# Performance work log

Hardware: AMD Instinct MI355X
Metric: run time of the kernel (lower is better)

## Reference

```python
import jax, jax.numpy as jnp
import numpy as np
import math

B_, CIN, CH, COUT, H_, W_ = 4, 96, 96, 96, 48, 48
DSTATE, DTRANK = 16, math.ceil(CH / 16)
DI = 2 * CH


def conv2d(x, w, b=None, groups=1):
    # x: NCHW, w: OIHW, 'same' padding for odd kernels
    p = (w.shape[-1] - 1) // 2
    y = jax.lax.conv_general_dilated(x, w, (1, 1), [(p, p), (p, p)],
                                     dimension_numbers=('NCHW', 'OIHW', 'NCHW'),
                                     feature_group_count=groups)
    return y if b is None else y + b[None, :, None, None]


def layernorm_last(x, g, b, eps=1e-5):
    mu = x.mean(-1, keepdims=True)
    v = jnp.mean((x - mu) ** 2, -1, keepdims=True)
    return (x - mu) * jax.lax.rsqrt(v + eps) * g + b


def selective_scan(u, delta, A, Bs, Cs, D):
    # u, delta: (B,K,Di,L); A: (K,Di,N); Bs, Cs: (B,K,N,L); D: (K,Di)
    dt = jnp.moveaxis(delta, -1, 0)  # (L,B,K,Di)
    ut = jnp.moveaxis(u, -1, 0)
    Bt = jnp.moveaxis(Bs, -1, 0)     # (L,B,K,N)
    Ct = jnp.moveaxis(Cs, -1, 0)
    N = A.shape[-1]

    def step(h, inp):
        d, uu, bb, cc = inp
        # h: (B,K,Di,N)
        h = h * jnp.exp(d[..., None] * A) + (d * uu)[..., None] * bb[:, :, None, :]
        y = jnp.einsum('bkdn,bkn->bkd', h, cc)
        return h, y

    step = jax.checkpoint(step)
    h0 = jnp.zeros(u.shape[:3] + (N,), u.dtype)
    _, ys = jax.lax.scan(step, h0, (dt, ut, Bt, Ct))
    return jnp.moveaxis(ys, 0, -1) + u * D[None, :, :, None]


def ss2d(x, in_w, cw, cb, xpw, dtw, dtb, A_log, Dp, ong, onb, ow):
    # x: (B,H,W,C) -> (B,H,W,C)
    B, H, W, C = x.shape
    Di = in_w.shape[0] // 2
    xi, z = jnp.split(x @ in_w.T, 2, -1)
    xc = jax.nn.silu(conv2d(jnp.transpose(xi, (0, 3, 1, 2)), cw, cb, groups=Di))
    L = H * W
    xf = xc.reshape(B, Di, L)
    xwh = jnp.transpose(xc, (0, 1, 3, 2)).reshape(B, Di, L)
    xh = jnp.stack([xf, xwh], 1)                      # (B,2,Di,L)
    xs = jnp.concatenate([xh, jnp.flip(xh, -1)], 1)   # (B,4,Di,L) 4-direction cross-scan
    xdbl = jnp.einsum('bkdl,kcd->bkcl', xs, xpw)
    R = dtw.shape[-1]
    N = A_log.shape[-1]
    dts, Bs, Cs = jnp.split(xdbl, [R, R + N], axis=2)
    delta = jax.nn.softplus(jnp.einsum('bkrl,kdr->bkdl', dts, dtw) + dtb[None, :, :, None])
    A = -jnp.exp(A_log.reshape(4, Di, N))
    oy = selective_scan(xs, delta, A, Bs, Cs, Dp.reshape(4, Di))  # (B,4,Di,L)
    inv = jnp.flip(oy[:, 2:4], -1)
    why = jnp.transpose(oy[:, 1].reshape(B, Di, W, H), (0, 1, 3, 2)).reshape(B, Di, L)
    invwhy = jnp.transpose(inv[:, 1].reshape(B, Di, W, H), (0, 1, 3, 2)).reshape(B, Di, L)
    y = oy[:, 0] + inv[:, 0] + why + invwhy           # (B,Di,L)
    y = layernorm_last(jnp.transpose(y, (0, 2, 1)).reshape(B, H, W, Di), ong, onb)
    return (y * jax.nn.silu(z)) @ ow.T


def crm(x, s1, s2, gw, gb, p1, p2):
    C = x.shape[1]
    uc = C // 2
    up = conv2d(x[:, :uc], s1)
    low = conv2d(x[:, uc:], s2)
    Y1 = conv2d(up, gw, gb, groups=2) + conv2d(up, p1)
    Y2 = jnp.concatenate([conv2d(low, p2), low], 1)
    out = jnp.concatenate([Y1, Y2], 1)                # (B,2C,H,W)
    out = jax.nn.softmax(out.mean((2, 3), keepdims=True), axis=1) * out
    o1, o2 = jnp.split(out, 2, 1)
    return o1 + o2


def _forward(x, conv1_w, conv1_b, bn_g, bn_b, lin_w, lin_b, dw1_w, dw1_b, dw2_w, dw2_b, ag1_w, ag1_b, ag2_w, ag2_b, ln_g, ln_b, sq1_w, sq2_w, gwc_w, gwc_b, pwc1_w, pwc2_w, fin_w, fin_b, ss_in_w, ss_conv_w, ss_conv_b, ss_xproj_w, ss_dt_w, ss_dt_b, ss_Alog, ss_D, ss_outn_g, ss_outn_b, ss_out_w):
    C = conv1_w.shape[0]
    # conv1x1 + BatchNorm(eval: running mean 0, var 1) + ReLU
    h = conv2d(x, conv1_w, conv1_b)
    h = jax.nn.relu(h * (bn_g * jax.lax.rsqrt(jnp.float32(1.0 + 1e-5)))[None, :, None, None] + bn_b[None, :, None, None])
    # token-wise linear over channels
    t = jnp.transpose(h, (0, 2, 3, 1)) @ lin_w.T + lin_b
    h = jnp.transpose(t, (0, 3, 1, 2))
    # branch 1: DWConv -> SiLU -> SS2D
    x1 = jax.nn.silu(conv2d(h, dw1_w, dw1_b, groups=C))
    x1 = ss2d(jnp.transpose(x1, (0, 2, 3, 1)), ss_in_w, ss_conv_w, ss_conv_b,
              ss_xproj_w, ss_dt_w, ss_dt_b, ss_Alog, ss_D, ss_outn_g, ss_outn_b, ss_out_w)
    x1 = jnp.transpose(x1, (0, 3, 1, 2))
    # branch 2: DWConv -> SiLU -> AttentionGate modulation
    x2 = jax.nn.silu(conv2d(h, dw2_w, dw2_b, groups=C))
    g = jax.nn.sigmoid(conv2d(jax.nn.relu(conv2d(x2, ag1_w, ag1_b)), ag2_w, ag2_b))
    y = x1 + x2 * g
    # per-pixel channel LayerNorm
    mu = y.mean(1, keepdims=True)
    v = jnp.mean((y - mu) ** 2, 1, keepdims=True)
    y = (y - mu) * jax.lax.rsqrt(v + 1e-5) * ln_g[None, :, None, None] + ln_b[None, :, None, None]
    y = crm(y, sq1_w, sq2_w, gwc_w, gwc_b, pwc1_w, pwc2_w)
    out = jnp.transpose(y, (0, 2, 3, 1)) @ fin_w.T + fin_b
    return jnp.transpose(out, (0, 3, 1, 2))


def setup_inputs():
    key = jax.random.key(0)

    def rnd(i, shape, s=0.02):
        return (jax.random.normal(jax.random.fold_in(key, i), shape) * s).astype(jnp.float32)

    CH2, N, R = CH // 2, DSTATE, DTRANK
    inp = dict(
        x=jax.random.normal(jax.random.fold_in(key, 0), (B_, CIN, H_, W_), jnp.float32),
        conv1_w=rnd(1, (CH, CIN, 1, 1)), conv1_b=jnp.zeros((CH,), jnp.float32),
        bn_g=jnp.ones((CH,), jnp.float32), bn_b=jnp.zeros((CH,), jnp.float32),
        lin_w=rnd(2, (CH, CH)), lin_b=jnp.zeros((CH,), jnp.float32),
        dw1_w=rnd(3, (CH, 1, 3, 3)), dw1_b=jnp.zeros((CH,), jnp.float32),
        dw2_w=rnd(4, (CH, 1, 3, 3)), dw2_b=jnp.zeros((CH,), jnp.float32),
        ag1_w=rnd(5, (CH2, CH, 1, 1)), ag1_b=jnp.zeros((CH2,), jnp.float32),
        ag2_w=rnd(6, (CH, CH2, 1, 1)), ag2_b=jnp.zeros((CH,), jnp.float32),
        ln_g=jnp.ones((CH,), jnp.float32), ln_b=jnp.zeros((CH,), jnp.float32),
        sq1_w=rnd(7, (CH // 4, CH2, 1, 1)), sq2_w=rnd(8, (CH // 4, CH2, 1, 1)),
        gwc_w=rnd(9, (CH, CH // 8, 3, 3)), gwc_b=jnp.zeros((CH,), jnp.float32),
        pwc1_w=rnd(10, (CH, CH // 4, 1, 1)), pwc2_w=rnd(11, (CH - CH // 4, CH // 4, 1, 1)),
        fin_w=rnd(12, (COUT, CH)), fin_b=jnp.zeros((COUT,), jnp.float32),
        ss_in_w=rnd(13, (2 * DI, CH)),
        ss_conv_w=rnd(14, (DI, 1, 3, 3)), ss_conv_b=jnp.zeros((DI,), jnp.float32),
        ss_xproj_w=rnd(15, (4, R + 2 * N, DI)),
        ss_dt_w=rnd(16, (4, DI, R), R ** -0.5),
    )
    dt = jnp.exp(jax.random.uniform(jax.random.fold_in(key, 17), (4, DI)) *
                 (math.log(0.1) - math.log(0.001)) + math.log(0.001))
    inp['ss_dt_b'] = (dt + jnp.log(-jnp.expm1(-dt))).astype(jnp.float32)
    inp['ss_Alog'] = jnp.tile(jnp.log(jnp.arange(1, DSTATE + 1, dtype=jnp.float32))[None, :], (4 * DI, 1))
    inp['ss_D'] = jnp.ones((4 * DI,), jnp.float32)
    inp['ss_outn_g'] = jnp.ones((DI,), jnp.float32)
    inp['ss_outn_b'] = jnp.zeros((DI,), jnp.float32)
    inp['ss_out_w'] = rnd(18, (CH, DI))
    return inp


def reference(x, conv1_w, conv1_b, bn_g, bn_b, lin_w, lin_b, dw1_w, dw1_b, dw2_w, dw2_b, ag1_w, ag1_b, ag2_w, ag2_b, ln_g, ln_b, sq1_w, sq2_w, gwc_w, gwc_b, pwc1_w, pwc2_w, fin_w, fin_b, ss_in_w, ss_conv_w, ss_conv_b, ss_xproj_w, ss_dt_w, ss_dt_b, ss_Alog, ss_D, ss_outn_g, ss_outn_b, ss_out_w):
    return _forward(x, conv1_w, conv1_b, bn_g, bn_b, lin_w, lin_b, dw1_w, dw1_b, dw2_w, dw2_b, ag1_w, ag1_b, ag2_w, ag2_b, ln_g, ln_b, sq1_w, sq2_w, gwc_w, gwc_b, pwc1_w, pwc2_w, fin_w, fin_b, ss_in_w, ss_conv_w, ss_conv_b, ss_xproj_w, ss_dt_w, ss_dt_b, ss_Alog, ss_D, ss_outn_g, ss_outn_b, ss_out_w)
```

## Files before the change

kernel.cpp:

```cpp
#include <hip/hip_runtime.h>
#include <hip/hip_bf16.h>

#define Bn   4
#define CHn  96
#define Hh   48
#define Ww   48
#define Ll   2304
#define Pp   9216
#define DIn  192
#define Nn   16
#define Rr   6
#define Sseg   32
#define SEGL   72
#define NCH     9
#define HSPLIT 884736

__device__ inline float siluf(float x){ return x / (1.0f + __expf(-x)); }
__device__ inline float sigmf(float x){ return 1.0f / (1.0f + __expf(-x)); }

__device__ inline int pix_of(int k, int l){
  if (k == 0) return l;
  if (k == 1) return (l % 48) * 48 + l / 48;
  if (k == 2) return Ll - 1 - l;
  int lr = Ll - 1 - l; return (lr % 48) * 48 + lr / 48;
}
__device__ inline int l_of(int k, int p){
  if (k == 0) return p;
  if (k == 1) return (p % 48) * 48 + p / 48;
  if (k == 2) return Ll - 1 - p;
  return Ll - 1 - ((p % 48) * 48 + p / 48);
}

__device__ inline float4* hptr(float* lo, float* hi, size_t idx){
  return (float4*)(idx < HSPLIT ? lo + idx : hi + (idx - HSPLIT));
}

struct TArgs {
  const float* s[14];
  float* d[14];
  int rows[14];
  int cols[14];
};
__global__ void k_tr(TArgs a){
  int id = blockIdx.y;
  int n = a.rows[id] * a.cols[id];
  int t = blockIdx.x * blockDim.x + threadIdx.x;
  if (t < n){
    int r = t / a.cols[id];
    int c = t - r * a.cols[id];
    a.d[id][c * a.rows[id] + r] = a.s[id][t];
  }
}

__global__ __launch_bounds__(256) void k_pre(const float* __restrict__ x, const float* __restrict__ w1T, const float* __restrict__ b1,
                      const float* __restrict__ bng, const float* __restrict__ bnb,
                      const float* __restrict__ linT, const float* __restrict__ lb,
                      float* __restrict__ hlin){
  __shared__ float xv[16][97];
  __shared__ float hv[16][97];
  int tid = threadIdx.x;
  int m = tid >> 4, t = tid & 15;
  int p0 = blockIdx.x * 16;
  int b = p0 / Ll; int pp0 = p0 - b * Ll;
  #pragma unroll
  for (int it = 0; it < 6; ++it){
    int e = it * 256 + tid; int c = e >> 4; int mm = e & 15;
    xv[mm][c] = x[((size_t)(b * CHn + c)) * Ll + pp0 + mm];
  }
  __syncthreads();
  float acc[6];
  #pragma unroll
  for (int j = 0; j < 6; ++j) acc[j] = 0.f;
  for (int i = 0; i < CHn; ++i){
    float xval = xv[m][i];
    #pragma unroll
    for (int j = 0; j < 6; ++j)
      acc[j] = fmaf(w1T[i * CHn + t + 16 * j], xval, acc[j]);
  }
  #pragma unroll
  for (int j = 0; j < 6; ++j){
    int c = t + 16 * j;
    float s = bng[c] * rsqrtf(1.0f + 1e-5f);
    hv[m][c] = fmaxf((acc[j] + b1[c]) * s + bnb[c], 0.f);
  }
  __syncthreads();
  float a2[6];
  #pragma unroll
  for (int j = 0; j < 6; ++j) a2[j] = lb[t + 16 * j];
  for (int i = 0; i < CHn; ++i){
    float hval = hv[m][i];
    #pragma unroll
    for (int j = 0; j < 6; ++j)
      a2[j] = fmaf(linT[i * CHn + t + 16 * j], hval, a2[j]);
  }
  int p = p0 + m;
  #pragma unroll
  for (int j = 0; j < 6; ++j)
    hlin[(size_t)p * CHn + t + 16 * j] = a2[j];
}

__global__ void k_dw(const float* __restrict__ hlin,
                     const float* __restrict__ dw1w, const float* __restrict__ dw1b,
                     const float* __restrict__ dw2w, const float* __restrict__ dw2b,
                     float* __restrict__ x1pre, float* __restrict__ x2){
  int t = blockIdx.x * 256 + threadIdx.x;
  if (t >= Pp * CHn) return;
  int c = t % CHn; int p = t / CHn; int b = p / Ll; int pp = p - b * Ll;
  int r = pp / Ww; int cx = pp - r * Ww;
  float a1 = dw1b[c], a2 = dw2b[c];
  for (int dy = -1; dy <= 1; ++dy){
    int ny = r + dy; if ((unsigned)ny >= Hh) continue;
    for (int dx = -1; dx <= 1; ++dx){
      int nx = cx + dx; if ((unsigned)nx >= Ww) continue;
      float v = hlin[(size_t)((b * Ll) + ny * Ww + nx) * CHn + c];
      int wi = c * 9 + (dy + 1) * 3 + (dx + 1);
      a1 = fmaf(dw1w[wi], v, a1);
      a2 = fmaf(dw2w[wi], v, a2);
    }
  }
  x1pre[t] = siluf(a1);
  x2[t]   = siluf(a2);
}

__global__ __launch_bounds__(256) void k_gate(const float* __restrict__ x2,
                       const float* __restrict__ ag1T, const float* __restrict__ ag1b,
                       const float* __restrict__ ag2T, const float* __restrict__ ag2b,
                       float* __restrict__ x2g){
  __shared__ float xv[16][97];
  __shared__ float rv[16][49];
  int tid = threadIdx.x;
  int m = tid >> 4, t = tid & 15;
  int p0 = blockIdx.x * 16;
  #pragma unroll
  for (int it = 0; it < 6; ++it){
    int e = it * 256 + tid; int mm = e / 96; int c = e - mm * 96;
    xv[mm][c] = x2[(size_t)(p0 + mm) * CHn + c];
  }
  __syncthreads();
  float a[3];
  #pragma unroll
  for (int jj = 0; jj < 3; ++jj) a[jj] = ag1b[t + 16 * jj];
  for (int i = 0; i < CHn; ++i){
    float xval = xv[m][i];
    #pragma unroll
    for (int jj = 0; jj < 3; ++jj)
      a[jj] = fmaf(ag1T[i * 48 + t + 16 * jj], xval, a[jj]);
  }
  #pragma unroll
  for (int jj = 0; jj < 3; ++jj) rv[m][t + 16 * jj] = fmaxf(a[jj], 0.f);
  __syncthreads();
  float a2[6];
  #pragma unroll
  for (int j = 0; j < 6; ++j) a2[j] = ag2b[t + 16 * j];
  for (int i = 0; i < 48; ++i){
    float rval = rv[m][i];
    #pragma unroll
    for (int j = 0; j < 6; ++j)
      a2[j] = fmaf(ag2T[i * CHn + t + 16 * j], rval, a2[j]);
  }
  int p = p0 + m;
  #pragma unroll
  for (int j = 0; j < 6; ++j){
    int c = t + 16 * j;
    x2g[(size_t)p * CHn + c] = xv[m][c] * sigmf(a2[j]);
  }
}

__global__ __launch_bounds__(256) void k_ssin(const float* __restrict__ x1pre, const float* __restrict__ inT,
                                              float* __restrict__ xi, float* __restrict__ z){
  __shared__ float Xs[32][17];
  __shared__ float Wsh[32][128];
  int tid = threadIdx.x;
  int mt = blockIdx.x % 576; int nt = blockIdx.x / 576;
  int p0 = mt * 16, n0 = nt * 128;
  int tx = tid & 15, ty = tid >> 4;
  float acc[8];
  #pragma unroll
  for (int j = 0; j < 8; ++j) acc[j] = 0.f;
  for (int kc = 0; kc < 96; kc += 32){
    #pragma unroll
    for (int it = 0; it < 2; ++it){
      int e = it * 256 + tid; int dd = e & 31; int m = e >> 5;
      Xs[dd][m] = x1pre[(size_t)(p0 + m) * CHn + kc + dd];
    }
    #pragma unroll
    for (int it = 0; it < 16; ++it){
      int e = it * 256 + tid; int n = e & 127; int dd = e >> 7;
      Wsh[dd][n] = inT[(size_t)(kc + dd) * 384 + n0 + n];
    }
    __syncthreads();
    #pragma unroll
    for (int dd = 0; dd < 32; ++dd){
      float xv = Xs[dd][ty];
      #pragma unroll
      for (int j = 0; j < 8; ++j)
        acc[j] = fmaf(xv, Wsh[dd][tx + 16 * j], acc[j]);
    }
    __syncthreads();
  }
  int p = p0 + ty;
  #pragma unroll
  for (int j = 0; j < 8; ++j){
    int n = n0 + tx + 16 * j;
    float v = acc[j];
    if (n < 192) xi[(size_t)p * DIn + n] = v;
    else         z [(size_t)p * DIn + (n - 192)] = v;
  }
}

__global__ void k_ssdw(const float* __restrict__ xi, const float* __restrict__ scw,
                       const float* __restrict__ scb, float* __restrict__ xc){
  int t = blockIdx.x * 256 + threadIdx.x;
  if (t >= Pp * DIn) return;
  int d = t % DIn; int p = t / DIn; int b = p / Ll; int pp = p - b * Ll;
  int r = pp / Ww; int cx = pp - r * Ww;
  float a = scb[d];
  for (int dy = -1; dy <= 1; ++dy){
    int ny = r + dy; if ((unsigned)ny >= Hh) continue;
    for (int dx = -1; dx <= 1; ++dx){
      int nx = cx + dx; if ((unsigned)nx >= Ww) continue;
      float v = xi[(size_t)((b * Ll) + ny * Ww + nx) * DIn + d];
      a = fmaf(scw[d * 9 + (dy + 1) * 3 + (dx + 1)], v, a);
    }
  }
  xc[t] = siluf(a);
}

__global__ __launch_bounds__(256) void k_xproj(const float* __restrict__ xc,
    const float* __restrict__ xpwT, float* __restrict__ part){
  __shared__ float Xs[32][17];
  __shared__ float Wsh[32][160];
  int tid = threadIdx.x;
  int mt = blockIdx.x / 6; int kc = (blockIdx.x - mt * 6) * 32;
  int p0g = mt * 16;
  int tx = tid & 15, ty = tid >> 4;
  const float* xbase = xc + (size_t)p0g * DIn + kc;
  #pragma unroll
  for (int it = 0; it < 2; ++it){
    int e = it * 256 + tid; int dd = e & 31; int m = e >> 5;
    Xs[dd][m] = xbase[(size_t)m * DIn + dd];
  }
  #pragma unroll
  for (int it = 0; it < 20; ++it){
    int e = it * 256 + tid; int dd = e / 160; int n = e - dd * 160;
    Wsh[dd][n] = (n < 152) ? xpwT[(size_t)(kc + dd) * 152 + n] : 0.f;
  }
  __syncthreads();
  float acc[10];
  #pragma unroll
  for (int j = 0; j < 10; ++j) acc[j] = 0.f;
  #pragma unroll
  for (int dd = 0; dd < 32; ++dd){
    float xv = Xs[dd][ty];
    #pragma unroll
    for (int j = 0; j < 10; ++j)
      acc[j] = fmaf(xv, Wsh[dd][tx + 16 * j], acc[j]);
  }
  float* pb = part + ((size_t)blockIdx.x * 16 + ty) * 152;
  #pragma unroll
  for (int j = 0; j < 10; ++j){
    int n = tx + 16 * j;
    if (n < 152) pb[n] = acc[j];
  }
}

__global__ void k_xred(const float* __restrict__ part, float* __restrict__ bc,
                       float* __restrict__ dtsG){
  int t = blockIdx.x * 256 + threadIdx.x;
  if (t >= Pp * 152) return;
  int p = t / 152, n = t - p * 152;
  int mt = p >> 4, m = p & 15;
  const float* pb = part + ((size_t)(mt * 6) * 16 + m) * 152 + n;
  float s = 0.f;
  #pragma unroll
  for (int kc = 0; kc < 6; ++kc) s += pb[(size_t)kc * 16 * 152];
  int b = p / Ll; int pp = p - b * Ll;
  int k = n / 38, jj = n - k * 38;
  int l = l_of(k, pp);
  if (jj < 6) dtsG[((size_t)((b * 4 + k) * Ll + l)) * 6 + jj] = s;
  else        bc [((size_t)((b * 4 + k) * Ll + l)) * 32 + (jj - 6)] = s;
}

__global__ void k_pack(const float* __restrict__ dtsG, const float* __restrict__ dtwT,
                       const float* __restrict__ dtb, const float* __restrict__ xc,
                       float* __restrict__ packed){
  int t = blockIdx.x * 256 + threadIdx.x;
  if (t >= 36864 * DIn) return;
  int d = t % DIn; int row = t / DIn;
  int bk = row / Ll; int l = row - bk * Ll;
  int k = bk & 3; int b = bk >> 2;
  const float* ds = dtsG + (size_t)row * 6;
  float a = dtb[k * DIn + d];
  #pragma unroll
  for (int r = 0; r < 6; ++r)
    a = fmaf(dtwT[r * 768 + k * DIn + d], ds[r], a);
  float dt = fmaxf(a, 0.f) + __logf(1.0f + __expf(-fabsf(a)));
  int pix = pix_of(k, l);
  float u = xc[((size_t)(b * Ll) + pix) * DIn + d];
  int unit = bk * 12 + (d >> 4);
  size_t base = ((size_t)unit * Ll + l) * 32 + (d & 15);
  packed[base]      = dt;
  packed[base + 16] = dt * u;
}


__global__ __launch_bounds__(64) void k_scanA(const float* __restrict__ packed, const float* __restrict__ bc,
                                              const float* __restrict__ Alog,
                                              float* __restrict__ hend, float* __restrict__ dtsum){
  int blk = blockIdx.x; int unit = blk >> 5; int seg = blk & 31;
  int g = unit % 12; int bk = unit / 12; int k = bk & 3;
  int lane = threadIdx.x; int ch = lane >> 2; int ns = lane & 3; int nb = ns * 4;
  int d = g * 16 + ch;
  const int arow = (k * DIn + d) * 16 + nb;
  float A0 = -__expf(Alog[arow + 0]);
  float A1 = -__expf(Alog[arow + 1]);
  float A2 = -__expf(Alog[arow + 2]);
  float A3 = -__expf(Alog[arow + 3]);
  float h0 = 0.f, h1 = 0.f, h2 = 0.f, h3 = 0.f, dacc = 0.f;

  const int l0 = seg * SEGL;
  const float* pbase = packed + ((size_t)unit * Ll + l0) * 32;
  const float* bbase = bc + ((size_t)(bk * Ll) + l0) * 32;

  __shared__ float pl[256];
  __shared__ float blA[128];

  float4 pn = *(const float4*)(pbase + lane * 4);
  float4 bn;
  if (lane < 32) bn = *(const float4*)(bbase + (size_t)(lane >> 2) * 32 + (lane & 3) * 4);
  *(float4*)&pl[lane * 4] = pn;
  if (lane < 32) *(float4*)&blA[lane * 4] = bn;
  __syncthreads();

  for (int cc = 0; cc < NCH; ++cc){
    bool more = (cc + 1 < NCH);
    if (more){
      pn = *(const float4*)(pbase + (cc + 1) * 256 + lane * 4);
      if (lane < 32) bn = *(const float4*)(bbase + (size_t)((cc + 1) * 8 + (lane >> 2)) * 32 + (lane & 3) * 4);
    }
    #pragma unroll
    for (int lp = 0; lp < 8; ++lp){
      float dt = pl[lp * 32 + ch];
      float du = pl[lp * 32 + 16 + ch];
      float4 Bv = *(const float4*)&blA[lp * 16 + nb];
      dacc += dt;
      h0 = fmaf(h0, __expf(dt * A0), du * Bv.x);
      h1 = fmaf(h1, __expf(dt * A1), du * Bv.y);
      h2 = fmaf(h2, __expf(dt * A2), du * Bv.z);
      h3 = fmaf(h3, __expf(dt * A3), du * Bv.w);
    }
    __syncthreads();
    if (more){
      *(float4*)&pl[lane * 4] = pn;
      if (lane < 32) *(float4*)&blA[lane * 4] = bn;
    }
    __syncthreads();
  }
  size_t sb = (size_t)unit * Sseg + seg;
  *(float4*)&hend[sb * 256 + lane * 4] = make_float4(h0, h1, h2, h3);
  if (ns == 0) dtsum[sb * 16 + ch] = dacc;
}

__global__ __launch_bounds__(64) void k_comb(const float* __restrict__ Alog, const float* __restrict__ hend,
                                             const float* __restrict__ dtsum,
                                             float* __restrict__ hlo, float* __restrict__ hhi){
  int unit = blockIdx.x; int g = unit % 12; int bk = unit / 12; int k = bk & 3;
  int lane = threadIdx.x; int ch = lane >> 2; int ns = lane & 3; int nb = ns * 4;
  int d = g * 16 + ch;
  const int arow = (k * DIn + d) * 16 + nb;
  float A0 = -__expf(Alog[arow + 0]);
  float A1 = -__expf(Alog[arow + 1]);
  float A2 = -__expf(Alog[arow + 2]);
  float A3 = -__expf(Alog[arow + 3]);
  float h0 = 0.f, h1 = 0.f, h2 = 0.f, h3 = 0.f;
  for (int s = 0; s < Sseg; ++s){
    size_t sb = (size_t)unit * Sseg + s;
    *hptr(hlo, hhi, sb * 256 + lane * 4) = make_float4(h0, h1, h2, h3);
    float dsv = dtsum[sb * 16 + ch];
    float4 he = *(const float4*)&hend[sb * 256 + lane * 4];
    h0 = fmaf(h0, __expf(A0 * dsv), he.x);
    h1 = fmaf(h1, __expf(A1 * dsv), he.y);
    h2 = fmaf(h2, __expf(A2 * dsv), he.z);
    h3 = fmaf(h3, __expf(A3 * dsv), he.w);
  }
}

__global__ __launch_bounds__(64) void k_scanB(const float* __restrict__ packed, const float* __restrict__ bc,
                                              const float* __restrict__ Alog,
                                              float* __restrict__ hlo, float* __restrict__ hhi,
                                              float* __restrict__ ysum){
  int blk = blockIdx.x; int unit = blk >> 5; int seg = blk & 31;
  int g = unit % 12; int bk = unit / 12; int k = bk & 3; int b = bk >> 2;
  int lane = threadIdx.x; int ch = lane >> 2; int ns = lane & 3; int nb = ns * 4;
  int d = g * 16 + ch;
  const int arow = (k * DIn + d) * 16 + nb;
  float A0 = -__expf(Alog[arow + 0]);
  float A1 = -__expf(Alog[arow + 1]);
  float A2 = -__expf(Alog[arow + 2]);
  float A3 = -__expf(Alog[arow + 3]);
  size_t sb = (size_t)unit * Sseg + seg;
  float4 hi = *hptr(hlo, hhi, sb * 256 + lane * 4);
  float h0 = hi.x, h1 = hi.y, h2 = hi.z, h3 = hi.w;

  const int l0 = seg * SEGL;
  const float* pbase = packed + ((size_t)unit * Ll + l0) * 32;
  const float* bbase = bc + ((size_t)(bk * Ll) + l0) * 32;
  float* ybase = ysum + (size_t)(b * Ll) * DIn + d;

  __shared__ float pl[256];
  __shared__ float bl[256];

  float4 pn = *(const float4*)(pbase + lane * 4);
  float4 bn = *(const float4*)(bbase + lane * 4);
  *(float4*)&pl[lane * 4] = pn;
  *(float4*)&bl[lane * 4] = bn;
  __syncthreads();

  for (int cc = 0; cc < NCH; ++cc){
    bool more = (cc + 1 < NCH);
    if (more){
      pn = *(const float4*)(pbase + (cc + 1) * 256 + lane * 4);
      bn = *(const float4*)(bbase + (cc + 1) * 256 + lane * 4);
    }
    #pragma unroll
    for (int lp = 0; lp < 8; ++lp){
      float dt = pl[lp * 32 + ch];
      float du = pl[lp * 32 + 16 + ch];
      float4 Bv = *(const float4*)&bl[lp * 32 + nb];
      float4 Cv = *(const float4*)&bl[lp * 32 + 16 + nb];
      h0 = fmaf(h0, __expf(dt * A0), du * Bv.x);
      h1 = fmaf(h1, __expf(dt * A1), du * Bv.y);
      h2 = fmaf(h2, __expf(dt * A2), du * Bv.z);
      h3 = fmaf(h3, __expf(dt * A3), du * Bv.w);
      float yp = fmaf(h0, Cv.x, fmaf(h1, Cv.y, fmaf(h2, Cv.z, h3 * Cv.w)));
      yp += __shfl_xor(yp, 1);
      yp += __shfl_xor(yp, 2);
      if (ns == 0){
        int l = l0 + cc * 8 + lp;
        int pix = pix_of(k, l);
        atomicAdd(ybase + (size_t)pix * DIn, yp);
      }
    }
    __syncthreads();
    if (more){
      *(float4*)&pl[lane * 4] = pn;
      *(float4*)&bl[lane * 4] = bn;
    }
    __syncthreads();
  }
}

__device__ inline float block_sum_192(float* red, int d, float v){
  red[d] = v; __syncthreads();
  if (d < 96) red[d] += red[d + 96]; __syncthreads();
  if (d < 48) red[d] += red[d + 48]; __syncthreads();
  if (d < 24) red[d] += red[d + 24]; __syncthreads();
  if (d < 12) red[d] += red[d + 12]; __syncthreads();
  if (d < 6)  red[d] += red[d + 6];  __syncthreads();
  float tot = red[0] + red[1] + red[2] + red[3] + red[4] + red[5];
  __syncthreads();
  return tot;
}

__global__ __launch_bounds__(256) void k_combine(const float* __restrict__ ysum, const float* __restrict__ xc,
                          const float* __restrict__ z, const float* __restrict__ Dp,
                          const float* __restrict__ ong, const float* __restrict__ onb,
                          const float* __restrict__ owT, const float* __restrict__ x2g,
                          const float* __restrict__ lng, const float* __restrict__ lnb,
                          const float* __restrict__ sq1T, const float* __restrict__ sq2T,
                          float* __restrict__ ul){
  __shared__ float ygs[16 * 200];
  __shared__ float crs_s[16 * 104];
  __shared__ float Wsh[32][97];
  __shared__ float sqs[2304];
  int tid = threadIdx.x;
  int m = tid >> 4, t = tid & 15;
  int p = blockIdx.x * 16 + m;
  const float* yrow = ysum + (size_t)p * DIn;
  const float* urow = xc   + (size_t)p * DIn;
  const float* zrow = z    + (size_t)p * DIn;

  #pragma unroll
  for (int it = 0; it < 5; ++it){
    int e = it * 256 + tid;
    if (e < 1152) sqs[e] = sq1T[e];
  }
  #pragma unroll
  for (int it = 0; it < 5; ++it){
    int e = it * 256 + tid;
    if (e < 1152) sqs[1152 + e] = sq2T[e];
  }

  float yv[12];
  float s1 = 0.f;
  #pragma unroll
  for (int j = 0; j < 12; ++j){
    int d = t + 16 * j;
    float Ds = Dp[d] + Dp[192 + d] + Dp[384 + d] + Dp[576 + d];
    float v = fmaf(urow[d], Ds, yrow[d]);
    yv[j] = v; s1 += v;
  }
  #pragma unroll
  for (int mk = 1; mk < 16; mk <<= 1) s1 += __shfl_xor(s1, mk, 16);
  float mu = s1 * (1.f / 192.f);
  float s2 = 0.f;
  #pragma unroll
  for (int j = 0; j < 12; ++j){ float dv = yv[j] - mu; s2 += dv * dv; }
  #pragma unroll
  for (int mk = 1; mk < 16; mk <<= 1) s2 += __shfl_xor(s2, mk, 16);
  float rstd = rsqrtf(s2 * (1.f / 192.f) + 1e-5f);
  #pragma unroll
  for (int j = 0; j < 12; ++j){
    int d = t + 16 * j;
    float yn = (yv[j] - mu) * rstd * ong[d] + onb[d];
    float zv = zrow[d];
    ygs[m * 200 + d] = yn * (zv * sigmf(zv));
  }
  __syncthreads();

  float acc[6];
  #pragma unroll
  for (int jj = 0; jj < 6; ++jj) acc[jj] = 0.f;
  for (int kc = 0; kc < 192; kc += 32){
    #pragma unroll
    for (int it = 0; it < 12; ++it){
      int e = it * 256 + tid; int dd = e / 96; int n = e - dd * 96;
      Wsh[dd][n] = owT[(size_t)(kc + dd) * 96 + n];
    }
    __syncthreads();
    const float* yg = &ygs[m * 200 + kc];
    #pragma unroll
    for (int dd = 0; dd < 32; ++dd){
      float xv = yg[dd];
      #pragma unroll
      for (int jj = 0; jj < 6; ++jj)
        acc[jj] = fmaf(xv, Wsh[dd][t + 16 * jj], acc[jj]);
    }
    __syncthreads();
  }

  float sv[6]; float s3 = 0.f;
  #pragma unroll
  for (int jj = 0; jj < 6; ++jj){
    int c = t + 16 * jj;
    sv[jj] = acc[jj] + x2g[(size_t)p * CHn + c];
    s3 += sv[jj];
  }
  #pragma unroll
  for (int mk = 1; mk < 16; mk <<= 1) s3 += __shfl_xor(s3, mk, 16);
  float mu2 = s3 * (1.f / 96.f);
  float s4 = 0.f;
  #pragma unroll
  for (int jj = 0; jj < 6; ++jj){ float dv = sv[jj] - mu2; s4 += dv * dv; }
  #pragma unroll
  for (int mk = 1; mk < 16; mk <<= 1) s4 += __shfl_xor(s4, mk, 16);
  float rstd2 = rsqrtf(s4 * (1.f / 96.f) + 1e-5f);
  #pragma unroll
  for (int jj = 0; jj < 6; ++jj){
    int c = t + 16 * jj;
    crs_s[m * 104 + c] = (sv[jj] - mu2) * rstd2 * lng[c] + lnb[c];
  }
  __syncthreads();

  const float* cr = &crs_s[m * 104];
  #pragma unroll
  for (int jj = 0; jj < 3; ++jj){
    int o = t + 16 * jj;
    float a = 0.f;
    if (o < 24){
      for (int i = 0; i < 48; ++i) a = fmaf(sqs[i * 24 + o], cr[i], a);
    } else {
      int oo = o - 24;
      for (int i = 0; i < 48; ++i) a = fmaf(sqs[1152 + i * 24 + oo], cr[48 + i], a);
    }
    ul[(size_t)p * 48 + o] = a;
  }
}

__global__ __launch_bounds__(256) void k_y(const float* __restrict__ ul, const float* __restrict__ gwcT,
                    const float* __restrict__ gwcb, const float* __restrict__ pwc1T,
                    const float* __restrict__ pwc2T, float* __restrict__ Ybig){
  __shared__ float uls[3 * 18 * 48];
  int tid = threadIdx.x;
  int m = tid >> 4, t = tid & 15;
  int blk = blockIdx.x;
  int b = blk / 144; int rem = blk - b * 144;
  int r = rem / 3; int chunk = rem - r * 3;
  int cx0 = chunk * 16;
  for (int e = tid; e < 3 * 18 * 48; e += 256){
    int ch = e % 48; int rc = e / 48;
    int col = rc % 18; int row = rc / 18;
    int gr = r - 1 + row; int gc = cx0 - 1 + col;
    float v = 0.f;
    if ((unsigned)gr < Hh && (unsigned)gc < Ww)
      v = ul[((size_t)(b * Ll + gr * Ww + gc)) * 48 + ch];
    uls[e] = v;
  }
  __syncthreads();
  int p = b * Ll + r * Ww + cx0 + m;
  const float* u1 = &uls[(1 * 18 + m + 1) * 48];
  float* yout = Ybig + (size_t)p * 192;
  #pragma unroll 1
  for (int j = 0; j < 6; ++j){
    int oc = t + 16 * j;
    int grp = oc / 48;
    float acc = gwcb[oc];
    #pragma unroll 1
    for (int k9 = 0; k9 < 9; ++k9){
      int dy = k9 / 3; int dx = k9 - dy * 3;
      const float* un = &uls[((dy * 18) + m + dx) * 48 + grp * 12];
      const float* wrow = gwcT + k9 * 96 + oc;
      #pragma unroll
      for (int i = 0; i < 12; ++i)
        acc = fmaf(wrow[i * 864], un[i], acc);
    }
    #pragma unroll
    for (int i = 0; i < 24; ++i) acc = fmaf(pwc1T[i * 96 + oc], u1[i], acc);
    yout[oc] = acc;
  }
  #pragma unroll 1
  for (int j = 6; j < 12; ++j){
    int oc = t + 16 * j;
    float acc;
    if (oc < 168){
      int o2 = oc - 96; acc = 0.f;
      #pragma unroll
      for (int i = 0; i < 24; ++i) acc = fmaf(pwc2T[i * 72 + o2], u1[24 + i], acc);
    } else {
      acc = u1[24 + oc - 168];
    }
    yout[oc] = acc;
  }
}

__global__ void k_csum(const float* __restrict__ Ybig, float* __restrict__ csum_p){
  int b = blockIdx.x / 144; int ch = blockIdx.x - b * 144;
  int t = threadIdx.x;
  if (t >= 192) return;
  float acc = 0.f;
  const float* base = Ybig + (size_t)(b * Ll + ch * 16) * 192 + t;
  #pragma unroll
  for (int i = 0; i < 16; ++i) acc += base[(size_t)i * 192];
  csum_p[(size_t)blockIdx.x * 192 + t] = acc;
}

__global__ void k_softmax(const float* __restrict__ csum_p, float* __restrict__ wsm){
  int b = blockIdx.x; int t = threadIdx.x;
  __shared__ float red[192];
  float m = 0.f;
  for (int cc = 0; cc < 144; ++cc) m += csum_p[(size_t)(b * 144 + cc) * 192 + t];
  m *= (1.f / 2304.f);
  red[t] = m; __syncthreads();
  if (t < 96) red[t] = fmaxf(red[t], red[t + 96]); __syncthreads();
  if (t < 48) red[t] = fmaxf(red[t], red[t + 48]); __syncthreads();
  if (t < 24) red[t] = fmaxf(red[t], red[t + 24]); __syncthreads();
  if (t < 12) red[t] = fmaxf(red[t], red[t + 12]); __syncthreads();
  if (t < 6)  red[t] = fmaxf(red[t], red[t + 6]);  __syncthreads();
  float mx = fmaxf(fmaxf(fmaxf(red[0], red[1]), fmaxf(red[2], red[3])), fmaxf(red[4], red[5]));
  __syncthreads();
  float e = __expf(m - mx);
  float s = block_sum_192(red, t, e);
  wsm[b * 192 + t] = e / s;
}

__global__ __launch_bounds__(256) void k_final(const float* __restrict__ Ybig, const float* __restrict__ wsm,
                        const float* __restrict__ finT, const float* __restrict__ finb,
                        float* __restrict__ out){
  __shared__ float ys[16][193];
  __shared__ float ov[16][97];
  __shared__ float wv[192];
  int tid = threadIdx.x;
  int m = tid >> 4, t = tid & 15;
  int p0 = blockIdx.x * 16;
  int b = p0 / Ll; int pp0 = p0 - b * Ll;
  if (tid < 192) wv[tid] = wsm[b * 192 + tid];
  #pragma unroll
  for (int it = 0; it < 12; ++it){
    int e = it * 256 + tid; int mm = e / 192; int c = e - mm * 192;
    ys[mm][c] = Ybig[(size_t)(p0 + mm) * 192 + c];
  }
  __syncthreads();
  #pragma unroll
  for (int j = 0; j < 6; ++j){
    int c = t + 16 * j;
    ov[m][c] = wv[c] * ys[m][c] + wv[96 + c] * ys[m][96 + c];
  }
  __syncthreads();
  float res[6];
  #pragma unroll
  for (int j = 0; j < 6; ++j) res[j] = finb[t + 16 * j];
  for (int i = 0; i < 96; ++i){
    float oval = ov[m][i];
    #pragma unroll
    for (int j = 0; j < 6; ++j)
      res[j] = fmaf(finT[i * 96 + t + 16 * j], oval, res[j]);
  }
  #pragma unroll
  for (int j = 0; j < 6; ++j) ys[m][t + 16 * j] = res[j];
  __syncthreads();
  #pragma unroll
  for (int it = 0; it < 6; ++it){
    int e = it * 256 + tid; int c = e >> 4; int mm = e & 15;
    out[((size_t)(b * CHn + c)) * Ll + pp0 + mm] = ys[mm][c];
  }
}

extern "C" void kernel_launch(void* const* d_in, const int* in_sizes, int n_in,
                              void* d_out, int out_size, void* d_ws, size_t ws_size,
                              hipStream_t stream) {
  const float* x     = (const float*)d_in[0];
  const float* w1    = (const float*)d_in[1];
  const float* b1    = (const float*)d_in[2];
  const float* bng   = (const float*)d_in[3];
  const float* bnb   = (const float*)d_in[4];
  const float* linw  = (const float*)d_in[5];
  const float* linb  = (const float*)d_in[6];
  const float* dw1w  = (const float*)d_in[7];
  const float* dw1b  = (const float*)d_in[8];
  const float* dw2w  = (const float*)d_in[9];
  const float* dw2b  = (const float*)d_in[10];
  const float* ag1w  = (const float*)d_in[11];
  const float* ag1b  = (const float*)d_in[12];
  const float* ag2w  = (const float*)d_in[13];
  const float* ag2b  = (const float*)d_in[14];
  const float* lng   = (const float*)d_in[15];
  const float* lnb   = (const float*)d_in[16];
  const float* sq1w  = (const float*)d_in[17];
  const float* sq2w  = (const float*)d_in[18];
  const float* gwcw  = (const float*)d_in[19];
  const float* gwcb  = (const float*)d_in[20];
  const float* pwc1w = (const float*)d_in[21];
  const float* pwc2w = (const float*)d_in[22];
  const float* finw  = (const float*)d_in[23];
  const float* finb  = (const float*)d_in[24];
  const float* inw   = (const float*)d_in[25];
  const float* scw   = (const float*)d_in[26];
  const float* scb   = (const float*)d_in[27];
  const float* xpw   = (const float*)d_in[28];
  const float* dtw   = (const float*)d_in[29];
  const float* dtb   = (const float*)d_in[30];
  const float* Alog  = (const float*)d_in[31];
  const float* Dp    = (const float*)d_in[32];
  const float* ong   = (const float*)d_in[33];
  const float* onb   = (const float*)d_in[34];
  const float* oww   = (const float*)d_in[35];

  float* ws = (float*)d_ws;
  float* hlin   = ws + 0;
  float* dtsum  = ws + 442368;
  float* x1pre  = ws + 884736;
  float* x2     = ws + 1769472;
  float* x2g    = ws + 2654208;
  float* xibuf  = ws + 3538944;
  float* zbuf   = ws + 5308416;
  float* xcbuf  = ws + 7077888;
  float* packed = ws + 8847360;
  float* bcbuf  = ws + 23003136;
  float* ysum   = ws + 24182784;
  float* wT     = ws + 25952256;

  float* dtsG    = x2;
  float* hend    = xibuf;
  float* hinitlo = x1pre;
  float* hinithi = x2;
  float* ulb     = hlin;
  float* Ybig    = xibuf;
  float* csum_p  = x1pre;
  float* wsmb    = x1pre + 110592;
  float* part    = packed;

  float* w1T   = wT + 0;
  float* linT  = wT + 9216;
  float* ag1T  = wT + 18432;
  float* ag2T  = wT + 23040;
  float* inT   = wT + 27648;
  float* owT   = wT + 64512;
  float* pwc1T = wT + 82944;
  float* pwc2T = wT + 85248;
  float* finT  = wT + 86976;
  float* sq1T  = wT + 96192;
  float* sq2T  = wT + 97344;
  float* gwcT  = wT + 98496;
  float* dtwT  = wT + 108864;
  float* xpwT  = wT + 113472;

  TArgs ta;
  const float* srcs[14] = {w1, linw, ag1w, ag2w, inw, oww, pwc1w, pwc2w, finw, sq1w, sq2w, gwcw, dtw, xpw};
  float* dsts[14]       = {w1T, linT, ag1T, ag2T, inT, owT, pwc1T, pwc2T, finT, sq1T, sq2T, gwcT, dtwT, xpwT};
  int rows[14] = {96, 96, 48, 96, 384, 96, 96, 72, 96, 24, 24, 96, 768, 152};
  int cols[14] = {96, 96, 96, 48, 96, 192, 24, 24, 96, 48, 48, 108, 6, 192};
  for (int i = 0; i < 14; ++i){ ta.s[i] = srcs[i]; ta.d[i] = dsts[i]; ta.rows[i] = rows[i]; ta.cols[i] = cols[i]; }

  k_tr<<<dim3(144, 14), 256, 0, stream>>>(ta);
  k_pre<<<576, 256, 0, stream>>>(x, w1T, b1, bng, bnb, linT, linb, hlin);
  k_dw<<<(Pp * CHn) / 256, 256, 0, stream>>>(hlin, dw1w, dw1b, dw2w, dw2b, x1pre, x2);
  k_gate<<<576, 256, 0, stream>>>(x2, ag1T, ag1b, ag2T, ag2b, x2g);
  k_ssin<<<576 * 3, 256, 0, stream>>>(x1pre, inT, xibuf, zbuf);
  k_ssdw<<<(Pp * DIn) / 256, 256, 0, stream>>>(xibuf, scw, scb, xcbuf);
  k_xproj<<<576 * 6, 256, 0, stream>>>(xcbuf, xpwT, part);
  k_xred<<<(Pp * 152 + 255) / 256, 256, 0, stream>>>(part, bcbuf, dtsG);
  k_pack<<<(36864 * DIn) / 256, 256, 0, stream>>>(dtsG, dtwT, dtb, xcbuf, packed);
  hipMemsetAsync(ysum, 0, (size_t)1769472 * 4, stream);
  k_scanA<<<192 * Sseg, 64, 0, stream>>>(packed, bcbuf, Alog, hend, dtsum);
  k_comb<<<192, 64, 0, stream>>>(Alog, hend, dtsum, hinitlo, hinithi);
  k_scanB<<<192 * Sseg, 64, 0, stream>>>(packed, bcbuf, Alog, hinitlo, hinithi, ysum);
  k_combine<<<576, 256, 0, stream>>>(ysum, xcbuf, zbuf, Dp, ong, onb, owT, x2g, lng, lnb, sq1T, sq2T, ulb);
  k_y<<<576, 256, 0, stream>>>(ulb, gwcT, gwcb, pwc1T, pwc2T, Ybig);
  k_csum<<<576, 256, 0, stream>>>(Ybig, csum_p);
  k_softmax<<<4, 192, 0, stream>>>(csum_p, wsmb);
  k_final<<<576, 256, 0, stream>>>(Ybig, wsmb, finT, finb, (float*)d_out);
}
```

Baseline: 339.1 us.

## Split combine kernel into layernorm-gate, split-K out-projection, and final LN kernels

The fused k_combine kernel is replaced by three kernels. k_lngate does the per-pixel layernorm and SiLU gate with one wavefront per pixel. k_oproj does the 192->96 output projection split into two K halves across 1152 blocks, writing partial sums. k_finc adds the two partials plus the residual, then applies the second layernorm and the squeeze projections. The aim is more parallelism and less per-block serial work in the projection, at the cost of two extra launches and a round trip through global memory for the intermediates.

```diff
diff --git a/kernel.cpp b/kernel.cpp
--- a/kernel.cpp
+++ b/kernel.cpp
@@ -462,24 +462,91 @@
   return tot;
 }
 
-__global__ __launch_bounds__(256) void k_combine(const float* __restrict__ ysum, const float* __restrict__ xc,
-                          const float* __restrict__ z, const float* __restrict__ Dp,
-                          const float* __restrict__ ong, const float* __restrict__ onb,
-                          const float* __restrict__ owT, const float* __restrict__ x2g,
-                          const float* __restrict__ lng, const float* __restrict__ lnb,
-                          const float* __restrict__ sq1T, const float* __restrict__ sq2T,
-                          float* __restrict__ ul){
-  __shared__ float ygs[16 * 200];
+__global__ __launch_bounds__(256) void k_lngate(const float* __restrict__ ysum, const float* __restrict__ xc,
+                        const float* __restrict__ z, const float* __restrict__ Dp,
+                        const float* __restrict__ ong, const float* __restrict__ onb,
+                        float* __restrict__ ygb){
+  int tid = threadIdx.x;
+  int w = tid >> 6;
+  int l = tid & 63;
+  int p = blockIdx.x * 4 + w;
+  const float* yrow = ysum + (size_t)p * DIn;
+  const float* urow = xc   + (size_t)p * DIn;
+  const float* zrow = z    + (size_t)p * DIn;
+  float yv[3]; float s1 = 0.f;
+  #pragma unroll
+  for (int j = 0; j < 3; ++j){
+    int d = l + 64 * j;
+    float Ds = Dp[d] + Dp[192 + d] + Dp[384 + d] + Dp[576 + d];
+    float v = fmaf(urow[d], Ds, yrow[d]);
+    yv[j] = v; s1 += v;
+  }
+  #pragma unroll
+  for (int mk = 1; mk < 64; mk <<= 1) s1 += __shfl_xor(s1, mk, 64);
+  float mu = s1 * (1.f / 192.f);
+  float s2 = 0.f;
+  #pragma unroll
+  for (int j = 0; j < 3; ++j){ float dv = yv[j] - mu; s2 += dv * dv; }
+  #pragma unroll
+  for (int mk = 1; mk < 64; mk <<= 1) s2 += __shfl_xor(s2, mk, 64);
+  float rstd = rsqrtf(s2 * (1.f / 192.f) + 1e-5f);
+  #pragma unroll
+  for (int j = 0; j < 3; ++j){
+    int d = l + 64 * j;
+    float yn = (yv[j] - mu) * rstd * ong[d] + onb[d];
+    float zv = zrow[d];
+    ygb[(size_t)p * DIn + d] = yn * (zv * sigmf(zv));
+  }
+}
+
+__global__ __launch_bounds__(256) void k_oproj(const float* __restrict__ ygb, const float* __restrict__ owT,
+                       float* __restrict__ part2){
+  __shared__ float Xs[32][17];
+  __shared__ float Wsh[32][97];
+  int tid = threadIdx.x;
+  int mt = blockIdx.x >> 1; int kh = (blockIdx.x & 1) * 96;
+  int p0 = mt * 16;
+  int tx = tid & 15, ty = tid >> 4;
+  float acc[6];
+  #pragma unroll
+  for (int jj = 0; jj < 6; ++jj) acc[jj] = 0.f;
+  for (int kc = 0; kc < 96; kc += 32){
+    #pragma unroll
+    for (int it = 0; it < 2; ++it){
+      int e = it * 256 + tid; int dd = e & 31; int m = e >> 5;
+      Xs[dd][m] = ygb[(size_t)(p0 + m) * DIn + kh + kc + dd];
+    }
+    #pragma unroll
+    for (int it = 0; it < 12; ++it){
+      int e = it * 256 + tid; int dd = e / 96; int n = e - dd * 96;
+      Wsh[dd][n] = owT[(size_t)(kh + kc + dd) * 96 + n];
+    }
+    __syncthreads();
+    #pragma unroll
+    for (int dd = 0; dd < 32; ++dd){
+      float xv = Xs[dd][ty];
+      #pragma unroll
+      for (int jj = 0; jj < 6; ++jj)
+        acc[jj] = fmaf(xv, Wsh[dd][tx + 16 * jj], acc[jj]);
+    }
+    __syncthreads();
+  }
+  float* pb = part2 + ((size_t)blockIdx.x * 16 + ty) * 96;
+  #pragma unroll
+  for (int jj = 0; jj < 6; ++jj)
+    pb[tx + 16 * jj] = acc[jj];
+}
+
+__global__ __launch_bounds__(256) void k_finc(const float* __restrict__ part2, const float* __restrict__ x2g,
+                      const float* __restrict__ lng, const float* __restrict__ lnb,
+                      const float* __restrict__ sq1T, const float* __restrict__ sq2T,
+                      float* __restrict__ ul){
   __shared__ float crs_s[16 * 104];
-  __shared__ float Wsh[32][97];
   __shared__ float sqs[2304];
   int tid = threadIdx.x;
   int m = tid >> 4, t = tid & 15;
-  int p = blockIdx.x * 16 + m;
-  const float* yrow = ysum + (size_t)p * DIn;
-  const float* urow = xc   + (size_t)p * DIn;
-  const float* zrow = z    + (size_t)p * DIn;
-
+  int mt = blockIdx.x;
+  int p = mt * 16 + m;
   #pragma unroll
   for (int it = 0; it < 5; ++it){
     int e = it * 256 + tid;
@@ -490,61 +557,14 @@
     int e = it * 256 + tid;
     if (e < 1152) sqs[1152 + e] = sq2T[e];
   }
-
-  float yv[12];
-  float s1 = 0.f;
-  #pragma unroll
-  for (int j = 0; j < 12; ++j){
-    int d = t + 16 * j;
-    float Ds = Dp[d] + Dp[192 + d] + Dp[384 + d] + Dp[576 + d];
-    float v = fmaf(urow[d], Ds, yrow[d]);
-    yv[j] = v; s1 += v;
-  }
-  #pragma unroll
-  for (int mk = 1; mk < 16; mk <<= 1) s1 += __shfl_xor(s1, mk, 16);
-  float mu = s1 * (1.f / 192.f);
-  float s2 = 0.f;
-  #pragma unroll
-  for (int j = 0; j < 12; ++j){ float dv = yv[j] - mu; s2 += dv * dv; }
-  #pragma unroll
-  for (int mk = 1; mk < 16; mk <<= 1) s2 += __shfl_xor(s2, mk, 16);
-  float rstd = rsqrtf(s2 * (1.f / 192.f) + 1e-5f);
-  #pragma unroll
-  for (int j = 0; j < 12; ++j){
-    int d = t + 16 * j;
-    float yn = (yv[j] - mu) * rstd * ong[d] + onb[d];
-    float zv = zrow[d];
-    ygs[m * 200 + d] = yn * (zv * sigmf(zv));
-  }
-  __syncthreads();
-
-  float acc[6];
-  #pragma unroll
-  for (int jj = 0; jj < 6; ++jj) acc[jj] = 0.f;
-  for (int kc = 0; kc < 192; kc += 32){
-    #pragma unroll
-    for (int it = 0; it < 12; ++it){
-      int e = it * 256 + tid; int dd = e / 96; int n = e - dd * 96;
-      Wsh[dd][n] = owT[(size_t)(kc + dd) * 96 + n];
-    }
-    __syncthreads();
-    const float* yg = &ygs[m * 200 + kc];
-    #pragma unroll
-    for (int dd = 0; dd < 32; ++dd){
-      float xv = yg[dd];
-      #pragma unroll
-      for (int jj = 0; jj < 6; ++jj)
-        acc[jj] = fmaf(xv, Wsh[dd][t + 16 * jj], acc[jj]);
-    }
-    __syncthreads();
-  }
-
+  const float* pa = part2 + ((size_t)(mt * 2)     * 16 + m) * 96;
+  const float* pbp = part2 + ((size_t)(mt * 2 + 1) * 16 + m) * 96;
   float sv[6]; float s3 = 0.f;
   #pragma unroll
   for (int jj = 0; jj < 6; ++jj){
     int c = t + 16 * jj;
-    sv[jj] = acc[jj] + x2g[(size_t)p * CHn + c];
-    s3 += sv[jj];
+    float v = pa[c] + pbp[c] + x2g[(size_t)p * CHn + c];
+    sv[jj] = v; s3 += v;
   }
   #pragma unroll
   for (int mk = 1; mk < 16; mk <<= 1) s3 += __shfl_xor(s3, mk, 16);
@@ -561,7 +581,6 @@
     crs_s[m * 104 + c] = (sv[jj] - mu2) * rstd2 * lng[c] + lnb[c];
   }
   __syncthreads();
-
   const float* cr = &crs_s[m * 104];
   #pragma unroll
   for (int jj = 0; jj < 3; ++jj){
@@ -768,6 +787,8 @@
   float* csum_p  = x1pre;
   float* wsmb    = x1pre + 110592;
   float* part    = packed;
+  float* ygb     = packed;
+  float* part2   = packed + 1769472;
 
   float* w1T   = wT + 0;
   float* linT  = wT + 9216;
@@ -804,7 +825,9 @@
   k_scanA<<<192 * Sseg, 64, 0, stream>>>(packed, bcbuf, Alog, hend, dtsum);
   k_comb<<<192, 64, 0, stream>>>(Alog, hend, dtsum, hinitlo, hinithi);
   k_scanB<<<192 * Sseg, 64, 0, stream>>>(packed, bcbuf, Alog, hinitlo, hinithi, ysum);
-  k_combine<<<576, 256, 0, stream>>>(ysum, xcbuf, zbuf, Dp, ong, onb, owT, x2g, lng, lnb, sq1T, sq2T, ulb);
+  k_lngate<<<2304, 256, 0, stream>>>(ysum, xcbuf, zbuf, Dp, ong, onb, ygb);
+  k_oproj<<<1152, 256, 0, stream>>>(ygb, owT, part2);
+  k_finc<<<576, 256, 0, stream>>>(part2, x2g, lng, lnb, sq1T, sq2T, ulb);
   k_y<<<576, 256, 0, stream>>>(ulb, gwcT, gwcb, pwc1T, pwc2T, Ybig);
   k_csum<<<576, 256, 0, stream>>>(Ybig, csum_p);
   k_softmax<<<4, 192, 0, stream>>>(csum_p, wsmb);
```

After: 336.9 us. About the same (-0.7%).
